# Kernel optimization log

Measured on AMD Instinct MI355X. Metric: run time of the kernel, lower is better.

The kernel has to match this reference:

```python
import jax, jax.numpy as jnp
import numpy as np

B, C, S, K, HEADS, P = 2, 64, 112, 7, 4, 3
DH = C // HEADS

def _na_idx(L, k):
    # NATTEN-style clamped windows: each query attends to k in-bounds neighbors
    i = np.arange(L)
    s = np.clip(i - k // 2, 0, L - k)
    nbr = s[:, None] + np.arange(k)[None, :]      # (L,k) absolute neighbor index
    rel = nbr - i[:, None] + (k - 1)              # (L,k) rel-pos-bias index in [0,2k-2]
    return jnp.asarray(nbr), jnp.asarray(rel)

def _ln(x, g, b, eps=1e-5):
    m = jnp.mean(x, -1, keepdims=True)
    v = jnp.mean(jnp.square(x - m), -1, keepdims=True)
    return (x - m) * jax.lax.rsqrt(v + eps) * g + b

def _conv(x, w, b):
    y = jax.lax.conv_general_dilated(x, w, (1, 1), [(P // 2, P // 2)] * 2,
                                     dimension_numbers=('NCHW', 'OIHW', 'NCHW'))
    return jnp.transpose(y + b[None, :, None, None], (0, 2, 3, 1))  # NHWC

def setup_inputs():
    key = jax.random.key(0)
    ks = jax.random.split(key, 24)
    r = lambda i, shape, s=0.02: jax.random.normal(ks[i], shape, jnp.float32) * s
    return {
        'xq': jax.random.normal(ks[0], (B, C, S, S), jnp.float32),
        'xkv': jax.random.normal(ks[1], (B, C, S, S), jnp.float32),
        'conv_w_s': r(2, (C, C, P, P)), 'conv_b_s': r(3, (C,), 0.01),
        'conv_w_l': r(4, (C, C, P, P)), 'conv_b_l': r(5, (C,), 0.01),
        'g_s': jnp.ones((C,), jnp.float32), 'b_s': jnp.zeros((C,), jnp.float32),
        'g_l': jnp.ones((C,), jnp.float32), 'b_l': jnp.zeros((C,), jnp.float32),
        'Wq': r(6, (C, C)), 'bq': r(7, (C,), 0.01),
        'Wk': r(8, (C, C)), 'bk': r(9, (C,), 0.01),
        'Wv': r(10, (C, C)), 'bv': r(11, (C,), 0.01),
        'Wo': r(12, (C, C)), 'bo': r(13, (C,), 0.01),
        'rpb': r(14, (HEADS, 2 * K - 1, 2 * K - 1)),
        'g_n': jnp.ones((C,), jnp.float32), 'b_n': jnp.zeros((C,), jnp.float32),
        'W1': r(15, (C, 2 * C)), 'b1': r(16, (2 * C,), 0.01),
        'W2': r(17, (2 * C, C)), 'b2': r(18, (C,), 0.01),
    }

def reference(xq, xkv, conv_w_s, conv_b_s, conv_w_l, conv_b_l, g_s, b_s, g_l, b_l,
              Wq, bq, Wk, bk, Wv, bv, Wo, bo, rpb, g_n, b_n, W1, b1, W2, b2):
    emb_q = _conv(xq, conv_w_s, conv_b_s)     # (B,H,W,C) overlap patch embed (q branch)
    emb_kv = _conv(xkv, conv_w_l, conv_b_l)   # (B,H,W,C)
    Hh, Ww = emb_q.shape[1], emb_q.shape[2]
    qn = _ln(emb_q, g_s, b_s)
    kvn = _ln(emb_kv, g_l, b_l)
    q = (qn @ Wq + bq).reshape(B, Hh, Ww, HEADS, DH)
    k = (kvn @ Wk + bk).reshape(B, Hh, Ww, HEADS, DH)
    v = (kvn @ Wv + bv).reshape(B, Hh, Ww, HEADS, DH)
    ni, ri = _na_idx(Hh, K)
    nj, rj = _na_idx(Ww, K)

    def gather(t):  # (B,H,W,h,d) -> (B,H,W,K*K,h,d) neighborhood windows
        t = t[:, ni]                                 # (B,H,K,W,h,d)
        t = t[:, :, :, nj]                           # (B,H,K,W,K,h,d)
        t = jnp.transpose(t, (0, 1, 3, 2, 4, 5, 6))  # (B,H,W,K,K,h,d)
        return t.reshape(B, Hh, Ww, K * K, HEADS, DH)

    kg, vg = gather(k), gather(v)
    logits = jnp.einsum('bijhd,bijnhd->bhijn', q, kg) * (DH ** -0.5)
    bias = rpb[:, ri]                                # (h,H,K,2K-1)
    bias = bias[:, :, :, rj]                         # (h,H,K,W,K)
    bias = jnp.transpose(bias, (0, 1, 3, 2, 4)).reshape(HEADS, Hh, Ww, K * K)
    attn = jax.nn.softmax(logits + bias[None], axis=-1)
    out = jnp.einsum('bhijn,bijnhd->bijhd', attn, vg).reshape(B, Hh, Ww, C)
    att = out @ Wo + bo + emb_kv                     # residual with kv embedding
    x = _ln(att, g_n, b_n)
    x = jax.nn.gelu(x @ W1 + b1, approximate=False) @ W2 + b2 + att
    return jnp.transpose(x, (0, 3, 1, 2))            # (B,C,H,W)
```

## Files before the change

### kernel.cpp

```cpp
#include <hip/hip_runtime.h>
#include <math.h>

#define SS 112
#define HW (SS*SS)
#define NPIX (2*HW)

typedef __bf16 v8bf __attribute__((ext_vector_type(8)));
typedef short  v8s  __attribute__((ext_vector_type(8)));
typedef float  v4f  __attribute__((ext_vector_type(4)));

__device__ __forceinline__ unsigned short f2bf(float f){
  unsigned u = __builtin_bit_cast(unsigned, f);
  u = (u + 0x7fffu + ((u >> 16) & 1u)) >> 16;
  return (unsigned short)u;
}
__device__ __forceinline__ v8bf zero8(){
  v8s z = {0,0,0,0,0,0,0,0};
  return __builtin_bit_cast(v8bf, z);
}
__device__ __forceinline__ float gelu_exact(float x){
  return 0.5f * x * (1.0f + erff(x * 0.7071067811865476f));
}

__device__ __forceinline__ void pack_wconv(const float* __restrict__ w,
                                           unsigned short* __restrict__ WB, int idx){
  int lane = idx & 63, tslot = (idx >> 6) & 3, kk = idx >> 8;
  int tap = kk >> 1;
  int ic0 = ((kk & 1) << 5) + ((lane >> 4) << 3);
  int oc  = tslot*16 + (lane & 15);
  union { unsigned short u[8]; uint4 q; } pk;
  #pragma unroll
  for (int i = 0; i < 8; ++i) pk.u[i] = f2bf(w[(oc*64 + ic0 + i)*9 + tap]);
  ((uint4*)WB)[idx] = pk.q;
}
__device__ __forceinline__ void pack_wlin(const float* __restrict__ W,
                                          unsigned short* __restrict__ WB,
                                          int N, int idx){
  int lane = idx & 63;
  int tmp = idx >> 6;
  int tiles = N >> 4;
  int tslot = tmp % tiles;
  int kk = tmp / tiles;
  int k0 = kk*32 + ((lane >> 4) << 3);
  int oc = tslot*16 + (lane & 15);
  union { unsigned short u[8]; uint4 q; } pk;
  #pragma unroll
  for (int i = 0; i < 8; ++i) pk.u[i] = f2bf(W[(size_t)(k0 + i)*N + oc]);
  ((uint4*)WB)[idx] = pk.q;
}

__global__ __launch_bounds__(256) void k_prep_all(
    const float* __restrict__ cws, const float* __restrict__ cwl,
    const float* __restrict__ Wq, const float* __restrict__ Wk,
    const float* __restrict__ Wv, const float* __restrict__ Wo,
    const float* __restrict__ W1, const float* __restrict__ W2,
    const float* __restrict__ rpb,
    unsigned short* __restrict__ WBs, unsigned short* __restrict__ WBl,
    unsigned short* __restrict__ WBq, unsigned short* __restrict__ WBk,
    unsigned short* __restrict__ WBv, unsigned short* __restrict__ WBo,
    unsigned short* __restrict__ WB1, unsigned short* __restrict__ WB2,
    float* __restrict__ rpb2)
{
  const int blk = blockIdx.x, t = threadIdx.x;
  if      (blk < 18) pack_wconv(cws, WBs, blk*256 + t);
  else if (blk < 36) pack_wconv(cwl, WBl, (blk-18)*256 + t);
  else if (blk < 38) pack_wlin(Wq, WBq, 64,  (blk-36)*256 + t);
  else if (blk < 40) pack_wlin(Wk, WBk, 64,  (blk-38)*256 + t);
  else if (blk < 42) pack_wlin(Wv, WBv, 64,  (blk-40)*256 + t);
  else if (blk < 44) pack_wlin(Wo, WBo, 64,  (blk-42)*256 + t);
  else if (blk < 48) pack_wlin(W1, WB1, 128, (blk-44)*256 + t);
  else if (blk < 52) pack_wlin(W2, WB2, 64,  (blk-48)*256 + t);
  else {
    int idx = (blk-52)*256 + t;
    if (idx < 4*169) rpb2[idx] = rpb[idx] * 1.4426950408889634f;
  }
}

__global__ __launch_bounds__(256) void k_prep_x2(const float* __restrict__ xq,
                                                 const float* __restrict__ xkv,
                                                 unsigned short* __restrict__ xTq,
                                                 unsigned short* __restrict__ xTkv){
  __shared__ float tile[64][68];
  const int t = threadIdx.x;
  const int inst = blockIdx.x >= (NPIX/64) ? 1 : 0;
  const float* x = inst ? xkv : xq;
  unsigned short* xT = inst ? xTkv : xTq;
  const int base = (blockIdx.x - inst*(NPIX/64)) * 64;
  const int b = base / HW;
  const int r0 = base - b*HW;
  {
    const int c = t >> 2, xo = (t & 3) << 4;
    const float* src = x + ((size_t)(b*64 + c))*HW + r0 + xo;
    float4 v0 = ((const float4*)src)[0];
    float4 v1 = ((const float4*)src)[1];
    float4 v2 = ((const float4*)src)[2];
    float4 v3 = ((const float4*)src)[3];
    float* dst = &tile[c][xo];
    ((float4*)dst)[0] = v0; ((float4*)dst)[1] = v1;
    ((float4*)dst)[2] = v2; ((float4*)dst)[3] = v3;
  }
  __syncthreads();
  {
    const int px = t >> 2, co = (t & 3) << 4;
    union { unsigned short u[16]; uint4 q[2]; } pk;
    #pragma unroll
    for (int i = 0; i < 16; ++i) pk.u[i] = f2bf(tile[co + i][px]);
    uint4* dst = (uint4*)(xT + ((size_t)(base + px))*64 + co);
    dst[0] = pk.q[0]; dst[1] = pk.q[1];
  }
}

__global__ __launch_bounds__(256) void k_conv_all(
    const unsigned short* __restrict__ xTq, const unsigned short* __restrict__ xTkv,
    const unsigned short* __restrict__ WBs, const unsigned short* __restrict__ WBl,
    const float* __restrict__ cbs, const float* __restrict__ g_s, const float* __restrict__ b_s,
    const float* __restrict__ cbl, const float* __restrict__ g_l, const float* __restrict__ b_l,
    const unsigned short* __restrict__ WBq, const float* __restrict__ bq_,
    const unsigned short* __restrict__ WBk, const float* __restrict__ bk_,
    const unsigned short* __restrict__ WBv, const float* __restrict__ bv_,
    unsigned short* __restrict__ qb, unsigned short* __restrict__ kb,
    unsigned short* __restrict__ vT, float* __restrict__ emb)
{
  __shared__ unsigned short nlds[4][16*64];
  const int tid = threadIdx.x;
  const int wid = tid >> 6, l = tid & 63;
  const int g = l >> 4, c = l & 15;
  const int HALF = NPIX/64;
  const int inst = blockIdx.x >= HALF ? 1 : 0;
  const int P0 = ((blockIdx.x - inst*HALF)*4 + wid) * 16;

  const unsigned short* xT  = inst ? xTkv : xTq;
  const unsigned short* WBc = inst ? WBl : WBs;
  const float* cb    = inst ? cbl : cbs;
  const float* gamma = inst ? g_l : g_s;
  const float* beta  = inst ? b_l : b_s;

  const int p = P0 + c;
  const int b = p / HW, r = p - b*HW;
  const int py = r / SS, pxx = r - py*SS;
  const int pb64 = b*HW;

  float cbv[4], gv[4], bev[4];
  #pragma unroll
  for (int t = 0; t < 4; ++t){
    cbv[t] = cb[c + 16*t]; gv[t] = gamma[c + 16*t]; bev[t] = beta[c + 16*t];
  }

  v4f acc[4];
  #pragma unroll
  for (int t = 0; t < 4; ++t) acc[t] = (v4f){cbv[t], cbv[t], cbv[t], cbv[t]};

  const int icg = g << 3;
  #pragma unroll
  for (int kk = 0; kk < 18; ++kk){
    const int tap = kk >> 1;
    const int dy = tap/3 - 1, dx = tap - (tap/3)*3 - 1;
    const int icof = ((kk & 1) << 5) + icg;
    int yy = py + dy, xx = pxx + dx;
    bool ok = ((unsigned)yy < SS) && ((unsigned)xx < SS);
    v8bf a = zero8();
    if (ok) a = *(const v8bf*)(xT + ((size_t)(pb64 + yy*SS + xx))*64 + icof);
    #pragma unroll
    for (int t = 0; t < 4; ++t){
      v8bf bfr = *(const v8bf*)(WBc + ((size_t)((kk*4 + t)*64 + l))*8);
      acc[t] = __builtin_amdgcn_mfma_f32_16x16x32_bf16(a, bfr, acc[t], 0, 0, 0);
    }
  }

  if (inst){
    #pragma unroll
    for (int t = 0; t < 4; ++t)
      #pragma unroll
      for (int r2 = 0; r2 < 4; ++r2)
        emb[((size_t)(P0 + 4*g + r2))*64 + c + 16*t] = acc[t][r2];
  }

  {
    float mean[4], inv[4];
    #pragma unroll
    for (int r2 = 0; r2 < 4; ++r2){
      float s = acc[0][r2] + acc[1][r2] + acc[2][r2] + acc[3][r2];
      s += __shfl_xor(s, 1, 64); s += __shfl_xor(s, 2, 64);
      s += __shfl_xor(s, 4, 64); s += __shfl_xor(s, 8, 64);
      mean[r2] = s * (1.f/64.f);
      float d0 = acc[0][r2] - mean[r2], d1 = acc[1][r2] - mean[r2];
      float d2 = acc[2][r2] - mean[r2], d3 = acc[3][r2] - mean[r2];
      float vs = d0*d0 + d1*d1 + d2*d2 + d3*d3;
      vs += __shfl_xor(vs, 1, 64); vs += __shfl_xor(vs, 2, 64);
      vs += __shfl_xor(vs, 4, 64); vs += __shfl_xor(vs, 8, 64);
      inv[r2] = rsqrtf(vs * (1.f/64.f) + 1e-5f);
    }
    #pragma unroll
    for (int t = 0; t < 4; ++t){
      int c16 = 2*t + (c >> 3);
      #pragma unroll
      for (int r2 = 0; r2 < 4; ++r2){
        int row = 4*g + r2;
        float n = (acc[t][r2] - mean[r2]) * inv[r2] * gv[t] + bev[t];
        nlds[wid][row*64 + (((c16 ^ (row & 7)) << 3) | (c & 7))] = f2bf(n);
      }
    }
  }

  #pragma unroll
  for (int which = 0; which < 2; ++which){
    if (which == 1 && !inst) break;
    const unsigned short* WB = which ? WBv : (inst ? WBk : WBq);
    const float* bias        = which ? bv_ : (inst ? bk_ : bq_);

    float pb[4];
    #pragma unroll
    for (int t = 0; t < 4; ++t) pb[t] = bias[c + 16*t];
    v4f pa[4];
    #pragma unroll
    for (int t = 0; t < 4; ++t) pa[t] = (v4f){pb[t], pb[t], pb[t], pb[t]};

    #pragma unroll
    for (int kk = 0; kk < 2; ++kk){
      v8bf av = *(const v8bf*)(nlds[wid] + c*64 + (((kk*4 + g) ^ (c & 7)) << 3));
      #pragma unroll
      for (int t = 0; t < 4; ++t){
        v8bf bfr = *(const v8bf*)(WB + ((size_t)((kk*4 + t)*64 + l))*8);
        pa[t] = __builtin_amdgcn_mfma_f32_16x16x32_bf16(av, bfr, pa[t], 0, 0, 0);
      }
    }
    if (which == 0){
      unsigned short* outp = inst ? kb : qb;
      #pragma unroll
      for (int t = 0; t < 4; ++t)
        #pragma unroll
        for (int r2 = 0; r2 < 4; ++r2)
          outp[((size_t)(P0 + 4*g + r2))*64 + c + 16*t] = f2bf(pa[t][r2]);
    } else {
      #pragma unroll
      for (int t = 0; t < 4; ++t)
        #pragma unroll
        for (int r2 = 0; r2 < 4; ++r2)
          vT[(size_t)(c + 16*t)*NPIX + (P0 + 4*g + r2)] = f2bf(pa[t][r2]);
    }
  }
}

__global__ __launch_bounds__(256) void k_natten_mfma(
    const unsigned short* __restrict__ q, const unsigned short* __restrict__ k,
    const unsigned short* __restrict__ vT, const float* __restrict__ rpb2,
    unsigned short* __restrict__ out)
{
  const int l = threadIdx.x & 63;
  const int h = threadIdx.x >> 6;
  const int p0 = blockIdx.x * 16;
  const int b = p0 / HW, r0 = p0 - b*HW;
  const int i = r0 / SS, j0 = r0 - i*SS;
  const int c = l & 15, g = l >> 4;

  const int si = min(max(i - 3, 0), SS - 7);
  const int aj = (min(max(j0 - 3, 0), SS - 22)) & ~7;
  const int oi = si - i + 6;
  const int pbase = b*HW;

  const int j   = j0 + c;
  const int sjp = min(max(j - 3, 0), SS - 7);
  const int adj = 8*g + (aj - sjp);
  const int e8  = 8*g + (aj - j + 6);

  v8bf bq = zero8();
  if (g < 2) bq = *(const v8bf*)(q + (size_t)(p0 + c)*64 + h*16 + 8*g);

  float lt[14][4];
  const int arow = 8*(c >> 2) + (c & 3);
  #pragma unroll
  for (int tau = 0; tau < 14; ++tau){
    const int t = tau >> 1;
    int kpix = pbase + (si + t)*SS + aj + arow + 4*(tau & 1);
    kpix = min(kpix, NPIX - 1);
    v8bf ak = zero8();
    if (g < 2) ak = *(const v8bf*)(k + (size_t)kpix*64 + h*16 + 8*g);
    v4f a0 = {0.f,0.f,0.f,0.f};
    a0 = __builtin_amdgcn_mfma_f32_16x16x32_bf16(ak, bq, a0, 0, 0, 0);
    lt[tau][0]=a0[0]; lt[tau][1]=a0[1]; lt[tau][2]=a0[2]; lt[tau][3]=a0[3];
  }

  const float SC = 0.3606737602222409f;
  float mx = -3e38f;
  #pragma unroll
  for (int tau = 0; tau < 14; ++tau){
    const int t = tau >> 1;
    const float* bt = rpb2 + h*169 + (t + oi)*13;
    #pragma unroll
    for (int r = 0; r < 4; ++r){
      const int cc = 4*(tau & 1) + r;
      int rj = min(max(e8 + cc, 0), 12);
      float bias = bt[rj];
      bool valid = (unsigned)(adj + cc) <= 6u;
      float lg = fmaf(lt[tau][r], SC, bias);
      lt[tau][r] = valid ? lg : -1e30f;
      mx = fmaxf(mx, lt[tau][r]);
    }
  }
  mx = fmaxf(mx, __shfl_xor(mx, 16, 64));
  mx = fmaxf(mx, __shfl_xor(mx, 32, 64));
  float es = 0.f;
  #pragma unroll
  for (int tau = 0; tau < 14; ++tau)
    #pragma unroll
    for (int r = 0; r < 4; ++r){
      float p = exp2f(lt[tau][r] - mx);
      lt[tau][r] = p;
      es += p;
    }
  es += __shfl_xor(es, 16, 64);
  es += __shfl_xor(es, 32, 64);
  const float inv = 1.0f / es;

  const unsigned short* vrow = vT + (size_t)(h*16 + c)*NPIX;
  v4f oacc = {0.f,0.f,0.f,0.f};
  #pragma unroll
  for (int t = 0; t < 7; ++t){
    union { unsigned short u[8]; v8bf bf; } pa;
    #pragma unroll
    for (int r = 0; r < 4; ++r){
      pa.u[r]     = f2bf(lt[2*t][r]   * inv);
      pa.u[4 + r] = f2bf(lt[2*t+1][r] * inv);
    }
    int vpixb = pbase + (si + t)*SS + aj + 8*g;
    vpixb = min(vpixb, NPIX - 8);
    v8bf bv = *(const v8bf*)(vrow + vpixb);
    oacc = __builtin_amdgcn_mfma_f32_16x16x32_bf16(pa.bf, bv, oacc, 0, 0, 0);
  }

  #pragma unroll
  for (int r = 0; r < 4; ++r)
    out[(size_t)(p0 + 4*g + r)*64 + h*16 + c] = f2bf(oacc[r]);
}

__global__ __launch_bounds__(256) void k_out_mfma(
    const unsigned short* __restrict__ ao, const float* __restrict__ emb,
    const unsigned short* __restrict__ WBo, const float* __restrict__ bo,
    const float* __restrict__ gn, const float* __restrict__ bn,
    const unsigned short* __restrict__ WB1, const float* __restrict__ b1,
    const unsigned short* __restrict__ WB2, const float* __restrict__ b2,
    float* __restrict__ outp)
{
  __shared__ unsigned short ylds[4][16*64];
  __shared__ unsigned short hlds[4][16*128];
  const int tid = threadIdx.x;
  const int wid = tid >> 6, l = tid & 63;
  const int g = l >> 4, c = l & 15;
  const int P0 = (blockIdx.x*4 + wid) * 16;
  const int b = P0 / HW;
  const int ijb = P0 - b*HW;

  v4f att[4];
  #pragma unroll
  for (int t = 0; t < 4; ++t){
    float bb = bo[c + 16*t];
    #pragma unroll
    for (int r = 0; r < 4; ++r)
      att[t][r] = bb + emb[((size_t)(P0 + 4*g + r))*64 + c + 16*t];
  }
  #pragma unroll
  for (int kk = 0; kk < 2; ++kk){
    v8bf a = *(const v8bf*)(ao + (size_t)(P0 + c)*64 + kk*32 + 8*g);
    #pragma unroll
    for (int t = 0; t < 4; ++t){
      v8bf bfr = *(const v8bf*)(WBo + ((size_t)((kk*4 + t)*64 + l))*8);
      att[t] = __builtin_amdgcn_mfma_f32_16x16x32_bf16(a, bfr, att[t], 0, 0, 0);
    }
  }

  {
    float gv[4], bev[4];
    #pragma unroll
    for (int t = 0; t < 4; ++t){ gv[t] = gn[c + 16*t]; bev[t] = bn[c + 16*t]; }
    float mean[4], inv[4];
    #pragma unroll
    for (int r = 0; r < 4; ++r){
      float s = att[0][r] + att[1][r] + att[2][r] + att[3][r];
      s += __shfl_xor(s, 1, 64); s += __shfl_xor(s, 2, 64);
      s += __shfl_xor(s, 4, 64); s += __shfl_xor(s, 8, 64);
      mean[r] = s * (1.f/64.f);
      float d0 = att[0][r] - mean[r], d1 = att[1][r] - mean[r];
      float d2 = att[2][r] - mean[r], d3 = att[3][r] - mean[r];
      float vs = d0*d0 + d1*d1 + d2*d2 + d3*d3;
      vs += __shfl_xor(vs, 1, 64); vs += __shfl_xor(vs, 2, 64);
      vs += __shfl_xor(vs, 4, 64); vs += __shfl_xor(vs, 8, 64);
      inv[r] = rsqrtf(vs * (1.f/64.f) + 1e-5f);
    }
    #pragma unroll
    for (int t = 0; t < 4; ++t){
      int c16 = 2*t + (c >> 3);
      #pragma unroll
      for (int r = 0; r < 4; ++r){
        int row = 4*g + r;
        float n = (att[t][r] - mean[r]) * inv[r] * gv[t] + bev[t];
        ylds[wid][row*64 + (((c16 ^ (row & 7)) << 3) | (c & 7))] = f2bf(n);
      }
    }
  }

  v4f hc[8];
  #pragma unroll
  for (int tt = 0; tt < 8; ++tt){
    float bb = b1[c + 16*tt];
    hc[tt] = (v4f){bb,bb,bb,bb};
  }
  #pragma unroll
  for (int kk = 0; kk < 2; ++kk){
    v8bf a = *(const v8bf*)(ylds[wid] + c*64 + (((kk*4 + g) ^ (c & 7)) << 3));
    #pragma unroll
    for (int tt = 0; tt < 8; ++tt){
      v8bf bfr = *(const v8bf*)(WB1 + ((size_t)((kk*8 + tt)*64 + l))*8);
      hc[tt] = __builtin_amdgcn_mfma_f32_16x16x32_bf16(a, bfr, hc[tt], 0, 0, 0);
    }
  }
  #pragma unroll
  for (int tt = 0; tt < 8; ++tt){
    int chunk = 2*tt + (c >> 3);
    #pragma unroll
    for (int r = 0; r < 4; ++r){
      int row = 4*g + r;
      int swz = (chunk & 8) | ((chunk & 7) ^ (row & 7));
      hlds[wid][row*128 + swz*8 + (c & 7)] = f2bf(gelu_exact(hc[tt][r]));
    }
  }

  v4f xc[4];
  #pragma unroll
  for (int t = 0; t < 4; ++t){
    float bb = b2[c + 16*t];
    #pragma unroll
    for (int r = 0; r < 4; ++r)
      xc[t][r] = bb + att[t][r];
  }
  #pragma unroll
  for (int kk = 0; kk < 4; ++kk){
    int chunk = 4*kk + g;
    int swz = (chunk & 8) | ((chunk & 7) ^ (c & 7));
    v8bf a = *(const v8bf*)(hlds[wid] + c*128 + swz*8);
    #pragma unroll
    for (int t = 0; t < 4; ++t){
      v8bf bfr = *(const v8bf*)(WB2 + ((size_t)((kk*4 + t)*64 + l))*8);
      xc[t] = __builtin_amdgcn_mfma_f32_16x16x32_bf16(a, bfr, xc[t], 0, 0, 0);
    }
  }
  #pragma unroll
  for (int t = 0; t < 4; ++t)
    #pragma unroll
    for (int r = 0; r < 4; ++r)
      outp[((size_t)(b*64 + c + 16*t))*HW + ijb + 4*g + r] = xc[t][r];
}

extern "C" void kernel_launch(void* const* d_in, const int* in_sizes, int n_in,
                              void* d_out, int out_size, void* d_ws, size_t ws_size,
                              hipStream_t stream) {
  const float* xq  = (const float*)d_in[0];
  const float* xkv = (const float*)d_in[1];
  const float* cws = (const float*)d_in[2];
  const float* cbs = (const float*)d_in[3];
  const float* cwl = (const float*)d_in[4];
  const float* cbl = (const float*)d_in[5];
  const float* g_s = (const float*)d_in[6];
  const float* b_s = (const float*)d_in[7];
  const float* g_l = (const float*)d_in[8];
  const float* b_l = (const float*)d_in[9];
  const float* Wq  = (const float*)d_in[10];
  const float* bq  = (const float*)d_in[11];
  const float* Wk  = (const float*)d_in[12];
  const float* bk  = (const float*)d_in[13];
  const float* Wv  = (const float*)d_in[14];
  const float* bv  = (const float*)d_in[15];
  const float* Wo  = (const float*)d_in[16];
  const float* bo  = (const float*)d_in[17];
  const float* rpb = (const float*)d_in[18];
  const float* g_n = (const float*)d_in[19];
  const float* b_n = (const float*)d_in[20];
  const float* W1  = (const float*)d_in[21];
  const float* b1  = (const float*)d_in[22];
  const float* W2  = (const float*)d_in[23];
  const float* b2  = (const float*)d_in[24];

  unsigned short* xTq  = (unsigned short*)d_ws;
  unsigned short* xTkv = xTq  + (size_t)NPIX*64;
  unsigned short* WBs  = xTkv + (size_t)NPIX*64;
  unsigned short* WBl  = WBs  + 36864;
  unsigned short* WBq  = WBl  + 36864;
  unsigned short* WBk  = WBq  + 4096;
  unsigned short* WBv  = WBk  + 4096;
  unsigned short* WBo  = WBv  + 4096;
  unsigned short* WB1  = WBo  + 4096;
  unsigned short* WB2  = WB1  + 8192;
  unsigned short* qb   = WB2  + 8192;
  unsigned short* kb   = qb   + (size_t)NPIX*64;
  unsigned short* vT   = kb   + (size_t)NPIX*64;
  unsigned short* aob  = vT   + (size_t)NPIX*64;
  float* emb  = (float*)(aob + (size_t)NPIX*64);
  float* rpb2 = emb + (size_t)NPIX*64;

  hipLaunchKernelGGL(k_prep_all, dim3(55), dim3(256), 0, stream,
      cws, cwl, Wq, Wk, Wv, Wo, W1, W2, rpb,
      WBs, WBl, WBq, WBk, WBv, WBo, WB1, WB2, rpb2);

  hipLaunchKernelGGL(k_prep_x2, dim3(NPIX/32), dim3(256), 0, stream,
      xq, xkv, xTq, xTkv);

  hipLaunchKernelGGL(k_conv_all, dim3(NPIX/32), dim3(256), 0, stream,
      xTq, xTkv, WBs, WBl,
      cbs, g_s, b_s, cbl, g_l, b_l,
      WBq, bq, WBk, bk, WBv, bv,
      qb, kb, vT, emb);

  hipLaunchKernelGGL(k_natten_mfma, dim3(NPIX/16), dim3(256), 0, stream,
      qb, kb, vT, rpb2, aob);

  hipLaunchKernelGGL(k_out_mfma, dim3(NPIX/64), dim3(256), 0, stream,
      aob, emb, WBo, bo, g_n, b_n, WB1, b1, WB2, b2, (float*)d_out);
}
```

Measured before the change: 84.81 us.

## Merge prep kernels, use packed bf16 converts, fast GELU, simpler bias lookup

Folds the weight-packing kernel and the input-transpose kernel into one launch, so one kernel launch and its gap disappear. Replaces the software fp32-to-bf16 rounding with the hardware v_cvt_pk_bf16_f32 instruction throughout, and writes vT with vector stores. Swaps the exact erf GELU for a tanh-style exp2/rcp approximation, which drifts from the reference's exact GELU. In the attention kernel it drops the clamped bias index in favor of a precomputed base pointer into a padded buffer, and splits the max and sum reductions into four independent chains to shorten dependency latency.

```diff
diff --git a/kernel.cpp b/kernel.cpp
--- a/kernel.cpp
+++ b/kernel.cpp
@@ -14,12 +14,20 @@
   u = (u + 0x7fffu + ((u >> 16) & 1u)) >> 16;
   return (unsigned short)u;
 }
+__device__ __forceinline__ unsigned cvt_pk_bf16(float lo, float hi){
+  unsigned r;
+  asm("v_cvt_pk_bf16_f32 %0, %1, %2" : "=v"(r) : "v"(lo), "v"(hi));
+  return r;
+}
 __device__ __forceinline__ v8bf zero8(){
   v8s z = {0,0,0,0,0,0,0,0};
   return __builtin_bit_cast(v8bf, z);
 }
-__device__ __forceinline__ float gelu_exact(float x){
-  return 0.5f * x * (1.0f + erff(x * 0.7071067811865476f));
+__device__ __forceinline__ float gelu_fast(float x){
+  float u = fmaf(0.044715f*x, x, 1.0f);
+  float z = fminf(2.3021178f * x * u, 80.0f);
+  float s = exp2f(z);
+  return x * s * __builtin_amdgcn_rcpf(s + 1.0f);
 }
 
 __device__ __forceinline__ void pack_wconv(const float* __restrict__ w,
@@ -49,7 +57,8 @@
   ((uint4*)WB)[idx] = pk.q;
 }
 
-__global__ __launch_bounds__(256) void k_prep_all(
+__global__ __launch_bounds__(256) void k_prep(
+    const float* __restrict__ xq, const float* __restrict__ xkv,
     const float* __restrict__ cws, const float* __restrict__ cwl,
     const float* __restrict__ Wq, const float* __restrict__ Wk,
     const float* __restrict__ Wv, const float* __restrict__ Wo,
@@ -59,33 +68,31 @@
     unsigned short* __restrict__ WBq, unsigned short* __restrict__ WBk,
     unsigned short* __restrict__ WBv, unsigned short* __restrict__ WBo,
     unsigned short* __restrict__ WB1, unsigned short* __restrict__ WB2,
-    float* __restrict__ rpb2)
+    float* __restrict__ rpb2g,
+    unsigned short* __restrict__ xTq, unsigned short* __restrict__ xTkv)
 {
+  __shared__ float tile[64][68];
   const int blk = blockIdx.x, t = threadIdx.x;
-  if      (blk < 18) pack_wconv(cws, WBs, blk*256 + t);
-  else if (blk < 36) pack_wconv(cwl, WBl, (blk-18)*256 + t);
-  else if (blk < 38) pack_wlin(Wq, WBq, 64,  (blk-36)*256 + t);
-  else if (blk < 40) pack_wlin(Wk, WBk, 64,  (blk-38)*256 + t);
-  else if (blk < 42) pack_wlin(Wv, WBv, 64,  (blk-40)*256 + t);
-  else if (blk < 44) pack_wlin(Wo, WBo, 64,  (blk-42)*256 + t);
-  else if (blk < 48) pack_wlin(W1, WB1, 128, (blk-44)*256 + t);
-  else if (blk < 52) pack_wlin(W2, WB2, 64,  (blk-48)*256 + t);
-  else {
-    int idx = (blk-52)*256 + t;
-    if (idx < 4*169) rpb2[idx] = rpb[idx] * 1.4426950408889634f;
-  }
-}
-
-__global__ __launch_bounds__(256) void k_prep_x2(const float* __restrict__ xq,
-                                                 const float* __restrict__ xkv,
-                                                 unsigned short* __restrict__ xTq,
-                                                 unsigned short* __restrict__ xTkv){
-  __shared__ float tile[64][68];
-  const int t = threadIdx.x;
-  const int inst = blockIdx.x >= (NPIX/64) ? 1 : 0;
+  if (blk < 55){
+    if      (blk < 18) pack_wconv(cws, WBs, blk*256 + t);
+    else if (blk < 36) pack_wconv(cwl, WBl, (blk-18)*256 + t);
+    else if (blk < 38) pack_wlin(Wq, WBq, 64,  (blk-36)*256 + t);
+    else if (blk < 40) pack_wlin(Wk, WBk, 64,  (blk-38)*256 + t);
+    else if (blk < 42) pack_wlin(Wv, WBv, 64,  (blk-40)*256 + t);
+    else if (blk < 44) pack_wlin(Wo, WBo, 64,  (blk-42)*256 + t);
+    else if (blk < 48) pack_wlin(W1, WB1, 128, (blk-44)*256 + t);
+    else if (blk < 52) pack_wlin(W2, WB2, 64,  (blk-48)*256 + t);
+    else {
+      int idx = (blk-52)*256 + t;
+      if (idx < 4*169) rpb2g[idx] = rpb[idx] * 1.4426950408889634f;
+    }
+    return;
+  }
+  const int blk2 = blk - 55;
+  const int inst = blk2 >= (NPIX/64) ? 1 : 0;
   const float* x = inst ? xkv : xq;
   unsigned short* xT = inst ? xTkv : xTq;
-  const int base = (blockIdx.x - inst*(NPIX/64)) * 64;
+  const int base = (blk2 - inst*(NPIX/64)) * 64;
   const int b = base / HW;
   const int r0 = base - b*HW;
   {
@@ -194,10 +201,13 @@
     for (int t = 0; t < 4; ++t){
       int c16 = 2*t + (c >> 3);
       #pragma unroll
-      for (int r2 = 0; r2 < 4; ++r2){
-        int row = 4*g + r2;
-        float n = (acc[t][r2] - mean[r2]) * inv[r2] * gv[t] + bev[t];
-        nlds[wid][row*64 + (((c16 ^ (row & 7)) << 3) | (c & 7))] = f2bf(n);
+      for (int r2 = 0; r2 < 4; r2 += 2){
+        int row0 = 4*g + r2, row1 = row0 + 1;
+        float n0 = (acc[t][r2]   - mean[r2])   * inv[r2]   * gv[t] + bev[t];
+        float n1 = (acc[t][r2+1] - mean[r2+1]) * inv[r2+1] * gv[t] + bev[t];
+        unsigned w = cvt_pk_bf16(n0, n1);
+        nlds[wid][row0*64 + (((c16 ^ (row0 & 7)) << 3) | (c & 7))] = (unsigned short)(w & 0xffffu);
+        nlds[wid][row1*64 + (((c16 ^ (row1 & 7)) << 3) | (c & 7))] = (unsigned short)(w >> 16);
       }
     }
   }
@@ -229,21 +239,26 @@
       #pragma unroll
       for (int t = 0; t < 4; ++t)
         #pragma unroll
-        for (int r2 = 0; r2 < 4; ++r2)
-          outp[((size_t)(P0 + 4*g + r2))*64 + c + 16*t] = f2bf(pa[t][r2]);
+        for (int r2 = 0; r2 < 4; r2 += 2){
+          unsigned w = cvt_pk_bf16(pa[t][r2], pa[t][r2+1]);
+          outp[((size_t)(P0 + 4*g + r2))*64 + c + 16*t]     = (unsigned short)(w & 0xffffu);
+          outp[((size_t)(P0 + 4*g + r2+1))*64 + c + 16*t]   = (unsigned short)(w >> 16);
+        }
     } else {
       #pragma unroll
-      for (int t = 0; t < 4; ++t)
-        #pragma unroll
-        for (int r2 = 0; r2 < 4; ++r2)
-          vT[(size_t)(c + 16*t)*NPIX + (P0 + 4*g + r2)] = f2bf(pa[t][r2]);
+      for (int t = 0; t < 4; ++t){
+        uint2 w2;
+        w2.x = cvt_pk_bf16(pa[t][0], pa[t][1]);
+        w2.y = cvt_pk_bf16(pa[t][2], pa[t][3]);
+        *(uint2*)(vT + (size_t)(c + 16*t)*NPIX + (P0 + 4*g)) = w2;
+      }
     }
   }
 }
 
 __global__ __launch_bounds__(256) void k_natten_mfma(
     const unsigned short* __restrict__ q, const unsigned short* __restrict__ k,
-    const unsigned short* __restrict__ vT, const float* __restrict__ rpb2,
+    const unsigned short* __restrict__ vT, const float* __restrict__ rpb2g,
     unsigned short* __restrict__ out)
 {
   const int l = threadIdx.x & 63;
@@ -261,7 +276,7 @@
   const int j   = j0 + c;
   const int sjp = min(max(j - 3, 0), SS - 7);
   const int adj = 8*g + (aj - sjp);
-  const int e8  = 8*g + (aj - j + 6);
+  const float* bp = rpb2g + h*169 + oi*13 + (8*g + aj - j + 6);
 
   v8bf bq = zero8();
   if (g < 2) bq = *(const v8bf*)(q + (size_t)(p0 + c)*64 + h*16 + 8*g);
@@ -281,33 +296,32 @@
   }
 
   const float SC = 0.3606737602222409f;
-  float mx = -3e38f;
+  float mx4[4] = {-3e38f,-3e38f,-3e38f,-3e38f};
   #pragma unroll
   for (int tau = 0; tau < 14; ++tau){
     const int t = tau >> 1;
-    const float* bt = rpb2 + h*169 + (t + oi)*13;
     #pragma unroll
     for (int r = 0; r < 4; ++r){
       const int cc = 4*(tau & 1) + r;
-      int rj = min(max(e8 + cc, 0), 12);
-      float bias = bt[rj];
-      bool valid = (unsigned)(adj + cc) <= 6u;
+      float bias = bp[t*13 + cc];
       float lg = fmaf(lt[tau][r], SC, bias);
-      lt[tau][r] = valid ? lg : -1e30f;
-      mx = fmaxf(mx, lt[tau][r]);
-    }
-  }
+      lt[tau][r] = ((unsigned)(adj + cc) <= 6u) ? lg : -1e30f;
+      mx4[r] = fmaxf(mx4[r], lt[tau][r]);
+    }
+  }
+  float mx = fmaxf(fmaxf(mx4[0], mx4[1]), fmaxf(mx4[2], mx4[3]));
   mx = fmaxf(mx, __shfl_xor(mx, 16, 64));
   mx = fmaxf(mx, __shfl_xor(mx, 32, 64));
-  float es = 0.f;
+  float es4[4] = {0.f,0.f,0.f,0.f};
   #pragma unroll
   for (int tau = 0; tau < 14; ++tau)
     #pragma unroll
     for (int r = 0; r < 4; ++r){
       float p = exp2f(lt[tau][r] - mx);
       lt[tau][r] = p;
-      es += p;
-    }
+      es4[r] += p;
+    }
+  float es = (es4[0] + es4[1]) + (es4[2] + es4[3]);
   es += __shfl_xor(es, 16, 64);
   es += __shfl_xor(es, 32, 64);
   const float inv = 1.0f / es;
@@ -316,12 +330,11 @@
   v4f oacc = {0.f,0.f,0.f,0.f};
   #pragma unroll
   for (int t = 0; t < 7; ++t){
-    union { unsigned short u[8]; v8bf bf; } pa;
-    #pragma unroll
-    for (int r = 0; r < 4; ++r){
-      pa.u[r]     = f2bf(lt[2*t][r]   * inv);
-      pa.u[4 + r] = f2bf(lt[2*t+1][r] * inv);
-    }
+    union { unsigned w[4]; v8bf bf; } pa;
+    pa.w[0] = cvt_pk_bf16(lt[2*t][0]*inv,   lt[2*t][1]*inv);
+    pa.w[1] = cvt_pk_bf16(lt[2*t][2]*inv,   lt[2*t][3]*inv);
+    pa.w[2] = cvt_pk_bf16(lt[2*t+1][0]*inv, lt[2*t+1][1]*inv);
+    pa.w[3] = cvt_pk_bf16(lt[2*t+1][2]*inv, lt[2*t+1][3]*inv);
     int vpixb = pbase + (si + t)*SS + aj + 8*g;
     vpixb = min(vpixb, NPIX - 8);
     v8bf bv = *(const v8bf*)(vrow + vpixb);
@@ -329,8 +342,11 @@
   }
 
   #pragma unroll
-  for (int r = 0; r < 4; ++r)
-    out[(size_t)(p0 + 4*g + r)*64 + h*16 + c] = f2bf(oacc[r]);
+  for (int r = 0; r < 4; r += 2){
+    unsigned w = cvt_pk_bf16(oacc[r], oacc[r+1]);
+    out[(size_t)(p0 + 4*g + r)*64 + h*16 + c]     = (unsigned short)(w & 0xffffu);
+    out[(size_t)(p0 + 4*g + r+1)*64 + h*16 + c]   = (unsigned short)(w >> 16);
+  }
 }
 
 __global__ __launch_bounds__(256) void k_out_mfma(
@@ -390,10 +406,13 @@
     for (int t = 0; t < 4; ++t){
       int c16 = 2*t + (c >> 3);
       #pragma unroll
-      for (int r = 0; r < 4; ++r){
-        int row = 4*g + r;
-        float n = (att[t][r] - mean[r]) * inv[r] * gv[t] + bev[t];
-        ylds[wid][row*64 + (((c16 ^ (row & 7)) << 3) | (c & 7))] = f2bf(n);
+      for (int r = 0; r < 4; r += 2){
+        int row0 = 4*g + r, row1 = row0 + 1;
+        float n0 = (att[t][r]   - mean[r])   * inv[r]   * gv[t] + bev[t];
+        float n1 = (att[t][r+1] - mean[r+1]) * inv[r+1] * gv[t] + bev[t];
+        unsigned w = cvt_pk_bf16(n0, n1);
+        ylds[wid][row0*64 + (((c16 ^ (row0 & 7)) << 3) | (c & 7))] = (unsigned short)(w & 0xffffu);
+        ylds[wid][row1*64 + (((c16 ^ (row1 & 7)) << 3) | (c & 7))] = (unsigned short)(w >> 16);
       }
     }
   }
@@ -417,10 +436,13 @@
   for (int tt = 0; tt < 8; ++tt){
     int chunk = 2*tt + (c >> 3);
     #pragma unroll
-    for (int r = 0; r < 4; ++r){
-      int row = 4*g + r;
-      int swz = (chunk & 8) | ((chunk & 7) ^ (row & 7));
-      hlds[wid][row*128 + swz*8 + (c & 7)] = f2bf(gelu_exact(hc[tt][r]));
+    for (int r = 0; r < 4; r += 2){
+      int row0 = 4*g + r, row1 = row0 + 1;
+      int swz0 = (chunk & 8) | ((chunk & 7) ^ (row0 & 7));
+      int swz1 = (chunk & 8) | ((chunk & 7) ^ (row1 & 7));
+      unsigned w = cvt_pk_bf16(gelu_fast(hc[tt][r]), gelu_fast(hc[tt][r+1]));
+      hlds[wid][row0*128 + swz0*8 + (c & 7)] = (unsigned short)(w & 0xffffu);
+      hlds[wid][row1*128 + swz1*8 + (c & 7)] = (unsigned short)(w >> 16);
     }
   }
 
@@ -493,15 +515,13 @@
   unsigned short* kb   = qb   + (size_t)NPIX*64;
   unsigned short* vT   = kb   + (size_t)NPIX*64;
   unsigned short* aob  = vT   + (size_t)NPIX*64;
-  float* emb  = (float*)(aob + (size_t)NPIX*64);
-  float* rpb2 = emb + (size_t)NPIX*64;
-
-  hipLaunchKernelGGL(k_prep_all, dim3(55), dim3(256), 0, stream,
-      cws, cwl, Wq, Wk, Wv, Wo, W1, W2, rpb,
-      WBs, WBl, WBq, WBk, WBv, WBo, WB1, WB2, rpb2);
-
-  hipLaunchKernelGGL(k_prep_x2, dim3(NPIX/32), dim3(256), 0, stream,
-      xq, xkv, xTq, xTkv);
+  float* emb   = (float*)(aob + (size_t)NPIX*64);
+  float* rpb2a = emb + (size_t)NPIX*64;
+  float* rpb2g = rpb2a + 64;
+
+  hipLaunchKernelGGL(k_prep, dim3(55 + NPIX/32), dim3(256), 0, stream,
+      xq, xkv, cws, cwl, Wq, Wk, Wv, Wo, W1, W2, rpb,
+      WBs, WBl, WBq, WBk, WBv, WBo, WB1, WB2, rpb2g, xTq, xTkv);
 
   hipLaunchKernelGGL(k_conv_all, dim3(NPIX/32), dim3(256), 0, stream,
       xTq, xTkv, WBs, WBl,
@@ -510,7 +530,7 @@
       qb, kb, vT, emb);
 
   hipLaunchKernelGGL(k_natten_mfma, dim3(NPIX/16), dim3(256), 0, stream,
-      qb, kb, vT, rpb2, aob);
+      qb, kb, vT, rpb2g, aob);
 
   hipLaunchKernelGGL(k_out_mfma, dim3(NPIX/64), dim3(256), 0, stream,
       aob, emb, WBo, bo, g_n, b_n, WB1, b1, WB2, b2, (float*)d_out);
```

After: 75.01 us. -11.5%, faster.
